# Optimization experiments

Hardware: AMD Instinct MI355X
Metric: run time of the kernel (lower is better)

The kernel has to match this reference:

```python
import jax, jax.numpy as jnp
import numpy as np

N_NODES = 50000
N_EDGES = 640000
D_IN = 128
D_H1 = 128
D_H2 = 256
NEG_SLOPE = 0.2


def setup_inputs() -> dict:
    key = jax.random.key(0)
    ks = jax.random.split(key, 12)
    s = 1.0 / np.sqrt(D_IN)
    inp = {
        'x': jax.random.normal(ks[0], (N_NODES, D_IN), dtype=jnp.float32),
        'edge_index': jax.random.randint(ks[1], (2, N_EDGES), 0, N_NODES, dtype=jnp.int64),
        # GATv2 layer 1: 128 -> 128 (separate lin_l / lin_r, attention vec, residual proj, bias)
        'Wl1': jax.random.normal(ks[2], (D_IN, D_H1), dtype=jnp.float32) * s,
        'Wr1': jax.random.normal(ks[3], (D_IN, D_H1), dtype=jnp.float32) * s,
        'att1': jax.random.normal(ks[4], (D_H1,), dtype=jnp.float32) * s,
        'Wres1': jax.random.normal(ks[5], (D_IN, D_H1), dtype=jnp.float32) * s,
        'b1': jnp.zeros((D_H1,), dtype=jnp.float32),
        # GATv2 layer 2: 128 -> 256
        'Wl2': jax.random.normal(ks[6], (D_H1, D_H2), dtype=jnp.float32) * s,
        'Wr2': jax.random.normal(ks[7], (D_H1, D_H2), dtype=jnp.float32) * s,
        'att2': jax.random.normal(ks[8], (D_H2,), dtype=jnp.float32) * s,
        'Wres2': jax.random.normal(ks[9], (D_H1, D_H2), dtype=jnp.float32) * s,
        'b2': jnp.zeros((D_H2,), dtype=jnp.float32),
    }
    return inp


def _gatv2_layer(x, Wl, Wr, att, Wres, b, src, dst, n_nodes):
    """GATv2Conv (heads=1, residual=True, eval mode/no dropout).
    score e_ij = att . LeakyReLU(Wl x_src + Wr x_dst); softmax over incoming edges per dst;
    out_dst = sum_j alpha_ij * (Wl x_src) + residual + bias.
    """
    xl = x @ Wl                      # [N, F]
    xr = x @ Wr                      # [N, F]
    h = xl[src] + xr[dst]            # [E, F]  gather (irregular access)
    e = jax.nn.leaky_relu(h, NEG_SLOPE) @ att   # [E]
    # segment softmax over destination nodes
    m = jax.ops.segment_max(e, dst, num_segments=n_nodes)      # [N]
    w = jnp.exp(e - m[dst])                                     # [E]
    denom = jax.ops.segment_sum(w, dst, num_segments=n_nodes)   # [N]
    alpha = w / (denom[dst] + 1e-16)                             # [E]
    out = jax.ops.segment_sum(alpha[:, None] * xl[src], dst, num_segments=n_nodes)  # [N, F]
    return out + x @ Wres + b


def reference(x, edge_index, Wl1, Wr1, att1, Wres1, b1, Wl2, Wr2, att2, Wres2, b2):
    src = edge_index[0]
    dst = edge_index[1]
    h = _gatv2_layer(x, Wl1, Wr1, att1, Wres1, b1, src, dst, N_NODES)
    h = jax.nn.elu(h)
    out = _gatv2_layer(h, Wl2, Wr2, att2, Wres2, b2, src, dst, N_NODES)
    return out
```

## Files before the change

kernel.cpp:

```cpp
#include <hip/hip_runtime.h>

typedef unsigned short u16;
typedef unsigned int u32;
typedef __attribute__((ext_vector_type(8))) short bf16x8;
typedef __attribute__((ext_vector_type(4))) float f32x4;
typedef __attribute__((ext_vector_type(2))) float f32x2;

#define NN 50000
#define NE 640000

__device__ __forceinline__ float bfl(u32 u) { return __uint_as_float(u << 16); }
__device__ __forceinline__ float bfh(u32 u) { return __uint_as_float(u & 0xffff0000u); }
__device__ __forceinline__ float bf1(u16 v) { return __uint_as_float(((u32)v) << 16); }
__device__ __forceinline__ u16 f2bf(float f) {
  u32 u = __float_as_uint(f);
  u32 r = (u + 0x7fffu + ((u >> 16) & 1u)) >> 16;
  return (u16)r;
}

__device__ __forceinline__ f32x2 bc2(float s) { return (f32x2){s, s}; }
__device__ __forceinline__ f32x2 pkfma(f32x2 a, f32x2 b, f32x2 c) {
  return __builtin_elementwise_fma(a, b, c);
}
__device__ __forceinline__ f32x2 pkabs(f32x2 a) {
  return __builtin_elementwise_abs(a);
}

template <int CTRL>
__device__ __forceinline__ float dpp_add(float x) {
  int t = __builtin_amdgcn_update_dpp(0, __float_as_int(x), CTRL, 0xf, 0xf, true);
  return x + __int_as_float(t);
}

__device__ __forceinline__ void unpk2(uint4 v, f32x2* o) {
  o[0] = (f32x2){bfl(v.x), bfh(v.x)};
  o[1] = (f32x2){bfl(v.y), bfh(v.y)};
  o[2] = (f32x2){bfl(v.z), bfh(v.z)};
  o[3] = (f32x2){bfl(v.w), bfh(v.w)};
}

__global__ void probe_kernel(const u16* __restrict__ x, const int* __restrict__ ei,
                             int* __restrict__ flags) {
  __shared__ int s_f32, s_i32;
  if (threadIdx.x == 0) { s_f32 = 0; s_i32 = 0; }
  __syncthreads();
  int lf = 0, li = 0;
  for (int i = threadIdx.x; i < 1024; i += 256) {
    float v = bf1(x[i]);
    if (!(fabsf(v) < 1e8f)) lf = 1;
    if (ei[2 * i + 1] != 0) li = 1;
  }
  if (lf) s_f32 = 1;
  if (li) s_i32 = 1;
  __syncthreads();
  if (threadIdx.x == 0) {
    flags[0] = s_f32;
    flags[1] = s_i32 ? 0 : 1;
  }
}

__device__ __forceinline__ int edge_val(const int* __restrict__ w, long j, int i64) {
  return i64 ? w[2 * j] : w[j];
}

__global__ void count_kernel(const int* __restrict__ ei, const int* __restrict__ flags,
                             int* __restrict__ cnt, int E) {
  int e = blockIdx.x * blockDim.x + threadIdx.x;
  if (e >= E) return;
  int d = edge_val(ei, (long)E + e, flags[1]);
  if ((u32)d < (u32)NN) atomicAdd(&cnt[d], 1);
}

__global__ void scan_local(const int* __restrict__ cnt, int* __restrict__ excl,
                           int* __restrict__ bsum, int n) {
  __shared__ int sd[256];
  int t = threadIdx.x;
  int g = blockIdx.x * 256 + t;
  int v = (g < n) ? cnt[g] : 0;
  sd[t] = v;
  __syncthreads();
  for (int off = 1; off < 256; off <<= 1) {
    int x = (t >= off) ? sd[t - off] : 0;
    __syncthreads();
    sd[t] += x;
    __syncthreads();
  }
  int incl = sd[t];
  if (g < n) excl[g] = incl - v;
  if (t == 255) bsum[blockIdx.x] = incl;
}

__global__ void scan_totals(const int* __restrict__ bsum, int* __restrict__ boff, int nb) {
  __shared__ int sd[256];
  int t = threadIdx.x;
  int v = (t < nb) ? bsum[t] : 0;
  sd[t] = v;
  __syncthreads();
  for (int off = 1; off < 256; off <<= 1) {
    int x = (t >= off) ? sd[t - off] : 0;
    __syncthreads();
    sd[t] += x;
    __syncthreads();
  }
  if (t < nb) boff[t] = sd[t] - v;
}

__global__ void scan_add(const int* __restrict__ excl, const int* __restrict__ boff,
                         const int* __restrict__ cnt, int* __restrict__ rowptr,
                         int* __restrict__ fillp, int n) {
  int g = blockIdx.x * 256 + threadIdx.x;
  if (g < n) {
    int e2 = excl[g] + boff[blockIdx.x];
    rowptr[g] = e2;
    fillp[g] = e2;
    if (g == n - 1) rowptr[n] = e2 + cnt[g];
  }
}

__global__ void fill_kernel(const int* __restrict__ ei, const int* __restrict__ flags,
                            int* __restrict__ fillp, int* __restrict__ col, int E) {
  int e = blockIdx.x * blockDim.x + threadIdx.x;
  if (e >= E) return;
  int i64 = flags[1];
  int s = edge_val(ei, (long)e, i64);
  int d = edge_val(ei, (long)E + e, i64);
  if ((u32)d >= (u32)NN) return;
  int p = atomicAdd(&fillp[d], 1);
  col[p] = ((u32)s < (u32)NN) ? s : 0;
}

__global__ void transpose_w(const void* W0, const void* W1, const void* W2,
                            const void* W3, const void* W4, const void* W5,
                            u16* T0, u16* T1, u16* T2, u16* T3, u16* T4, u16* T5,
                            const int* __restrict__ flags) {
  int y = blockIdx.y;
  int M = (y < 3) ? 128 : 256;
  int flat = blockIdx.x * 256 + threadIdx.x;
  if (flat >= M * 128) return;
  int j = flat >> 7;
  int k = flat & 127;
  const void* W = (y == 0) ? W0 : (y == 1) ? W1 : (y == 2) ? W2 : (y == 3) ? W3 : (y == 4) ? W4 : W5;
  u16* T = (y == 0) ? T0 : (y == 1) ? T1 : (y == 2) ? T2 : (y == 3) ? T3 : (y == 4) ? T4 : T5;
  u16 v;
  if (flags[0])
    v = f2bf(((const float*)W)[(size_t)k * M + j]);
  else
    v = ((const u16*)W)[(size_t)k * M + j];
  T[(size_t)j * 128 + k] = v;
}

#define LSTR 136
__global__ __launch_bounds__(256) void gemm3_mfma(
    const void* __restrict__ X,
    const u16* __restrict__ Wta, const u16* __restrict__ Wtb, const u16* __restrict__ Wtc,
    const void* __restrict__ bias,
    u16* __restrict__ Ya, u16* __restrict__ Yb, u16* __restrict__ Yc,
    const int* __restrict__ flags, int x_follows, int N, int M) {
  __shared__ __align__(16) u16 Xs[64 * LSTR];
  __shared__ __align__(16) u16 Bs[128 * LSTR];
  const int K = 128;
  int t = threadIdx.x;
  int lane = t & 63;
  int w = t >> 6;
  int n0g = blockIdx.x * 64;
  int c0 = blockIdx.z * 128;
  int F32X = x_follows ? flags[0] : 0;
  const u16* Wt = (blockIdx.y == 0) ? Wta : ((blockIdx.y == 1) ? Wtb : Wtc);
  u16* Y = (blockIdx.y == 0) ? Ya : ((blockIdx.y == 1) ? Yb : Yc);

  if (!F32X) {
    const u16* Xg = (const u16*)X;
    for (int it = 0; it < 4; ++it) {
      int i = t + 256 * it;
      int r = i >> 4, c8 = (i & 15) * 8;
      int n = n0g + r;
      uint4 v = make_uint4(0, 0, 0, 0);
      if (n < N) v = *(const uint4*)(Xg + (size_t)n * K + c8);
      *(uint4*)(Xs + r * LSTR + c8) = v;
    }
  } else {
    const float* Xg = (const float*)X;
    for (int it = 0; it < 4; ++it) {
      int i = t + 256 * it;
      int r = i >> 4, c8 = (i & 15) * 8;
      int n = n0g + r;
      uint4 pk = make_uint4(0, 0, 0, 0);
      if (n < N) {
        float4 f0 = *(const float4*)(Xg + (size_t)n * K + c8);
        float4 f1 = *(const float4*)(Xg + (size_t)n * K + c8 + 4);
        pk.x = (u32)f2bf(f0.x) | ((u32)f2bf(f0.y) << 16);
        pk.y = (u32)f2bf(f0.z) | ((u32)f2bf(f0.w) << 16);
        pk.z = (u32)f2bf(f1.x) | ((u32)f2bf(f1.y) << 16);
        pk.w = (u32)f2bf(f1.z) | ((u32)f2bf(f1.w) << 16);
      }
      *(uint4*)(Xs + r * LSTR + c8) = pk;
    }
  }
  for (int it = 0; it < 8; ++it) {
    int i = t + 256 * it;
    int j = i >> 4, k8 = (i & 15) * 8;
    uint4 v = *(const uint4*)(Wt + (size_t)(c0 + j) * K + k8);
    *(uint4*)(Bs + j * LSTR + k8) = v;
  }
  __syncthreads();

  int m0 = (w >> 1) * 32;
  int n0 = (w & 1) * 64;
  int l15 = lane & 15;
  int q8 = (lane >> 4) * 8;
  f32x4 acc[2][4];
#pragma unroll
  for (int i = 0; i < 2; ++i)
#pragma unroll
    for (int j = 0; j < 4; ++j) acc[i][j] = (f32x4){0.f, 0.f, 0.f, 0.f};

#pragma unroll
  for (int kc = 0; kc < 4; ++kc) {
    int ko = kc * 32 + q8;
    bf16x8 a[2], b[4];
#pragma unroll
    for (int i = 0; i < 2; ++i)
      a[i] = *(const bf16x8*)(Xs + (m0 + i * 16 + l15) * LSTR + ko);
#pragma unroll
    for (int j = 0; j < 4; ++j)
      b[j] = *(const bf16x8*)(Bs + (n0 + j * 16 + l15) * LSTR + ko);
#pragma unroll
    for (int i = 0; i < 2; ++i)
#pragma unroll
      for (int j = 0; j < 4; ++j)
        acc[i][j] = __builtin_amdgcn_mfma_f32_16x16x32_bf16(a[i], b[j], acc[i][j], 0, 0, 0);
  }
  __syncthreads();

  float bv[4] = {0.f, 0.f, 0.f, 0.f};
  if (blockIdx.y == 2) {
    int F32 = flags[0];
#pragma unroll
    for (int j = 0; j < 4; ++j) {
      int c = c0 + n0 + j * 16 + l15;
      bv[j] = F32 ? ((const float*)bias)[c] : bf1(((const u16*)bias)[c]);
    }
  }

  u16* Ct = Xs;
#pragma unroll
  for (int i = 0; i < 2; ++i)
#pragma unroll
    for (int j = 0; j < 4; ++j) {
      int col = n0 + j * 16 + l15;
      int rbase = m0 + i * 16 + (lane >> 4) * 4;
#pragma unroll
      for (int r = 0; r < 4; ++r)
        Ct[(rbase + r) * LSTR + col] = f2bf(acc[i][j][r] + bv[j]);
    }
  __syncthreads();

  for (int it = 0; it < 4; ++it) {
    int i = t + 256 * it;
    int r = i >> 4, c8 = (i & 15) * 8;
    int n = n0g + r;
    if (n < N) {
      uint4 v = *(const uint4*)(Ct + r * LSTR + c8);
      *(uint4*)(Y + (size_t)n * M + c0 + c8) = v;
    }
  }
}

template <int F, bool ELU, int GL>
__global__ __launch_bounds__(256) void gat_agg_kernel(
    const u16* __restrict__ xl, const u16* __restrict__ xr, const u16* __restrict__ res,
    const void* __restrict__ att, const int* __restrict__ rowptr, const int* __restrict__ col,
    void* __restrict__ out, const int* __restrict__ flags, int out_follows, int N) {
  constexpr int HEPL = F / GL;
  constexpr int HP = HEPL / 2;
  static_assert(HEPL == 8, "GL must be F/8");
  int tid = threadIdx.x;
  int gl = tid & (GL - 1);
  int node = blockIdx.x * (256 / GL) + (tid / GL);
  if (node >= N) return;
  int F32 = flags[0];
  int OF32 = out_follows ? F32 : 0;
  int base = gl * HEPL;

  f32x2 xr2[HP], att6[HP], att4[HP], acc2[HP];
  {
    uint4 xp = *(const uint4*)(xr + (size_t)node * F + base);
    unpk2(xp, xr2);
  }
  if (F32) {
    const float* af = (const float*)att + base;
#pragma unroll
    for (int p = 0; p < HP; ++p) {
      f32x2 a = (f32x2){af[2 * p], af[2 * p + 1]};
      att6[p] = a * 0.6f;
      att4[p] = a * 0.4f;
    }
  } else {
    f32x2 a2[HP];
    uint4 ap = *(const uint4*)((const u16*)att + base);
    unpk2(ap, a2);
#pragma unroll
    for (int p = 0; p < HP; ++p) {
      att6[p] = a2[p] * 0.6f;
      att4[p] = a2[p] * 0.4f;
    }
  }
#pragma unroll
  for (int p = 0; p < HP; ++p) acc2[p] = bc2(0.f);

  float m = -1e30f, l = 0.f;
  int beg = rowptr[node], end = rowptr[node + 1];
  int deg = end - beg;

  if (deg > 0) {
    int nit = (deg + 1) >> 1;
    int dm1 = deg - 1;
    auto ldc = [&](int j) -> int { return col[beg + min(j, dm1)]; };
    auto gat = [&](int c) -> uint4 { return *(const uint4*)(xl + (size_t)c * F + base); };

    int c4 = ldc(4), c5 = ldc(5);
    uint4 va = gat(ldc(0)), vb = gat(ldc(1)), vc = gat(ldc(2)), vd = gat(ldc(3));

    for (int t = 0; t < nit; ++t) {
      uint4 x0v = va, x1v = vb;
      int act1 = (2 * t + 1) < deg;
      va = vc; vb = vd;
      if (t + 2 < nit) { vc = gat(c4); vd = gat(c5); }
      if (t + 3 < nit) { c4 = ldc(2 * t + 6); c5 = ldc(2 * t + 7); }

      f32x2 x0[HP], x1[HP];
      unpk2(x0v, x0);
      unpk2(x1v, x1);
      f32x2 s0 = bc2(0.f), s1 = bc2(0.f);
#pragma unroll
      for (int p = 0; p < HP; ++p) {
        f32x2 h0 = x0[p] + xr2[p];
        f32x2 h1 = x1[p] + xr2[p];
        f32x2 ha0 = pkabs(h0);
        f32x2 ha1 = pkabs(h1);
        s0 = pkfma(att6[p], h0, s0);
        s1 = pkfma(att6[p], h1, s1);
        s0 = pkfma(att4[p], ha0, s0);
        s1 = pkfma(att4[p], ha1, s1);
      }
      float d0 = s0.x + s0.y;
      float d1 = s1.x + s1.y;
      d0 = dpp_add<0xB1>(d0);  d1 = dpp_add<0xB1>(d1);
      d0 = dpp_add<0x4E>(d0);  d1 = dpp_add<0x4E>(d1);
      d0 = dpp_add<0x141>(d0); d1 = dpp_add<0x141>(d1);
      d0 = dpp_add<0x140>(d0); d1 = dpp_add<0x140>(d1);
      if constexpr (GL == 32) {
        d0 += __shfl_xor(d0, 16, 64);
        d1 += __shfl_xor(d1, 16, 64);
      }

      float p0 = d0;
      float p1 = act1 ? d1 : -1e30f;
      float mn = fmaxf(m, fmaxf(p0, p1));
      float scl = __expf(m - mn);
      float w0 = __expf(p0 - mn);
      float w1 = __expf(p1 - mn);
      l = fmaf(l, scl, w0 + w1);
      f32x2 w0b = bc2(w0), w1b = bc2(w1), sclb = bc2(scl);
#pragma unroll
      for (int p = 0; p < HP; ++p)
        acc2[p] = pkfma(sclb, acc2[p], pkfma(w1b, x1[p], w0b * x0[p]));
      m = mn;
    }
  }

  float inv = 1.f / (l + 1e-16f);
  uint4 rp = *(const uint4*)(res + (size_t)node * F + base);
  f32x2 rv[HP];
  unpk2(rp, rv);
  f32x2 ov[HP];
  f32x2 invb = bc2(inv);
#pragma unroll
  for (int p = 0; p < HP; ++p) {
    f32x2 o = pkfma(acc2[p], invb, rv[p]);
    if (ELU) {
      o.x = (o.x > 0.f) ? o.x : (__expf(o.x) - 1.f);
      o.y = (o.y > 0.f) ? o.y : (__expf(o.y) - 1.f);
    }
    ov[p] = o;
  }
  if (OF32) {
    float* of = (float*)out + (size_t)node * F + base;
    float4 f0 = {ov[0].x, ov[0].y, ov[1].x, ov[1].y};
    float4 f1 = {ov[2].x, ov[2].y, ov[3].x, ov[3].y};
    *(float4*)of = f0;
    *(float4*)(of + 4) = f1;
  } else {
    u16* o16 = (u16*)out;
    uint4 pk;
    pk.x = (u32)f2bf(ov[0].x) | ((u32)f2bf(ov[0].y) << 16);
    pk.y = (u32)f2bf(ov[1].x) | ((u32)f2bf(ov[1].y) << 16);
    pk.z = (u32)f2bf(ov[2].x) | ((u32)f2bf(ov[2].y) << 16);
    pk.w = (u32)f2bf(ov[3].x) | ((u32)f2bf(ov[3].y) << 16);
    *(uint4*)(o16 + (size_t)node * F + base) = pk;
  }
}

extern "C" void kernel_launch(void* const* d_in, const int* in_sizes, int n_in,
                              void* d_out, int out_size, void* d_ws, size_t ws_size,
                              hipStream_t stream) {
  const u16* x16 = (const u16*)d_in[0];
  const int* ei = (const int*)d_in[1];
  const int N = NN, E = NE;

  char* ws = (char*)d_ws;
  size_t off = 0;
  auto alloc = [&](size_t bytes) -> void* {
    void* p = (void*)(ws + off);
    off += (bytes + 255) & ~(size_t)255;
    return p;
  };
  int* flags = (int*)alloc(2 * 4);
  int* cnt = (int*)alloc((size_t)N * 4);
  int* rowptr = (int*)alloc((size_t)(N + 1) * 4);
  int* fillp = (int*)alloc((size_t)N * 4);
  int* colb = (int*)alloc((size_t)E * 4);
  int* excl = (int*)alloc((size_t)N * 4);
  int* bsum = (int*)alloc(256 * 4);
  int* boff = (int*)alloc(256 * 4);
  u16* Wt1a = (u16*)alloc((size_t)128 * 128 * 2);
  u16* Wt1b = (u16*)alloc((size_t)128 * 128 * 2);
  u16* Wt1c = (u16*)alloc((size_t)128 * 128 * 2);
  u16* Wt2a = (u16*)alloc((size_t)256 * 128 * 2);
  u16* Wt2b = (u16*)alloc((size_t)256 * 128 * 2);
  u16* Wt2c = (u16*)alloc((size_t)256 * 128 * 2);
  u16* buf1 = (u16*)alloc((size_t)N * 256 * 2);
  u16* buf2 = (u16*)alloc((size_t)N * 256 * 2);
  u16* buf3 = (u16*)alloc((size_t)N * 256 * 2);
  u16* h1 = (u16*)alloc((size_t)N * 128 * 2);
  (void)ws_size; (void)n_in; (void)in_sizes; (void)out_size;

  int nb = (N + 255) / 256;

  probe_kernel<<<1, 256, 0, stream>>>(x16, ei, flags);
  hipMemsetAsync(cnt, 0, (size_t)N * 4, stream);
  count_kernel<<<(E + 255) / 256, 256, 0, stream>>>(ei, flags, cnt, E);
  scan_local<<<nb, 256, 0, stream>>>(cnt, excl, bsum, N);
  scan_totals<<<1, 256, 0, stream>>>(bsum, boff, nb);
  scan_add<<<nb, 256, 0, stream>>>(excl, boff, cnt, rowptr, fillp, N);
  fill_kernel<<<(E + 255) / 256, 256, 0, stream>>>(ei, flags, fillp, colb, E);
  transpose_w<<<dim3(128, 6), 256, 0, stream>>>(
      d_in[2], d_in[3], d_in[5], d_in[7], d_in[8], d_in[10],
      Wt1a, Wt1b, Wt1c, Wt2a, Wt2b, Wt2c, flags);

  int gx = (N + 63) / 64;
  gemm3_mfma<<<dim3(gx, 3, 1), 256, 0, stream>>>(
      d_in[0], Wt1a, Wt1b, Wt1c, d_in[6], buf1, buf2, buf3, flags, 1, N, 128);
  gat_agg_kernel<128, true, 16><<<(N + 15) / 16, 256, 0, stream>>>(
      buf1, buf2, buf3, d_in[4], rowptr, colb, h1, flags, 0, N);
  gemm3_mfma<<<dim3(gx, 3, 2), 256, 0, stream>>>(
      h1, Wt2a, Wt2b, Wt2c, d_in[11], buf1, buf2, buf3, flags, 0, N, 256);
  gat_agg_kernel<256, false, 32><<<(N + 7) / 8, 256, 0, stream>>>(
      buf1, buf2, buf3, d_in[9], rowptr, colb, d_out, flags, 1, N);
}
```

Baseline: 324.6 us.

## Merge setup kernels and loop output halves inside GEMM blocks

The probe kernel now also zeroes the degree counts, which removes a separate memset. The scan-totals kernel is folded into scan_add: each block reduces the preceding block sums itself. Both changes cut the number of launches. The layer-2 GEMM now handles both 128-column output halves in one block, loading the X tile once instead of launching a z-dimension of 2. This halves X tile reloads but gives fewer blocks and more serialized work per block.

```diff
diff --git a/kernel.cpp b/kernel.cpp
--- a/kernel.cpp
+++ b/kernel.cpp
@@ -39,23 +39,27 @@
   o[3] = (f32x2){bfl(v.w), bfh(v.w)};
 }
 
-__global__ void probe_kernel(const u16* __restrict__ x, const int* __restrict__ ei,
-                             int* __restrict__ flags) {
-  __shared__ int s_f32, s_i32;
-  if (threadIdx.x == 0) { s_f32 = 0; s_i32 = 0; }
-  __syncthreads();
-  int lf = 0, li = 0;
-  for (int i = threadIdx.x; i < 1024; i += 256) {
-    float v = bf1(x[i]);
-    if (!(fabsf(v) < 1e8f)) lf = 1;
-    if (ei[2 * i + 1] != 0) li = 1;
-  }
-  if (lf) s_f32 = 1;
-  if (li) s_i32 = 1;
-  __syncthreads();
-  if (threadIdx.x == 0) {
-    flags[0] = s_f32;
-    flags[1] = s_i32 ? 0 : 1;
+__global__ void probe_zero_kernel(const u16* __restrict__ x, const int* __restrict__ ei,
+                                  int* __restrict__ flags, int* __restrict__ cnt, int n) {
+  int g = blockIdx.x * 256 + threadIdx.x;
+  if (g < n) cnt[g] = 0;
+  if (blockIdx.x == 0) {
+    __shared__ int s_f32, s_i32;
+    if (threadIdx.x == 0) { s_f32 = 0; s_i32 = 0; }
+    __syncthreads();
+    int lf = 0, li = 0;
+    for (int i = threadIdx.x; i < 1024; i += 256) {
+      float v = bf1(x[i]);
+      if (!(fabsf(v) < 1e8f)) lf = 1;
+      if (ei[2 * i + 1] != 0) li = 1;
+    }
+    if (lf) s_f32 = 1;
+    if (li) s_i32 = 1;
+    __syncthreads();
+    if (threadIdx.x == 0) {
+      flags[0] = s_f32;
+      flags[1] = s_i32 ? 0 : 1;
+    }
   }
 }
 
@@ -90,27 +94,21 @@
   if (t == 255) bsum[blockIdx.x] = incl;
 }
 
-__global__ void scan_totals(const int* __restrict__ bsum, int* __restrict__ boff, int nb) {
+__global__ void scan_add(const int* __restrict__ excl, const int* __restrict__ bsum,
+                         const int* __restrict__ cnt, int* __restrict__ rowptr,
+                         int* __restrict__ fillp, int n, int nb) {
   __shared__ int sd[256];
   int t = threadIdx.x;
-  int v = (t < nb) ? bsum[t] : 0;
-  sd[t] = v;
+  sd[t] = (t < nb && t < (int)blockIdx.x) ? bsum[t] : 0;
   __syncthreads();
-  for (int off = 1; off < 256; off <<= 1) {
-    int x = (t >= off) ? sd[t - off] : 0;
-    __syncthreads();
-    sd[t] += x;
-    __syncthreads();
-  }
-  if (t < nb) boff[t] = sd[t] - v;
-}
-
-__global__ void scan_add(const int* __restrict__ excl, const int* __restrict__ boff,
-                         const int* __restrict__ cnt, int* __restrict__ rowptr,
-                         int* __restrict__ fillp, int n) {
-  int g = blockIdx.x * 256 + threadIdx.x;
+  for (int off = 128; off > 0; off >>= 1) {
+    if (t < off) sd[t] += sd[t + off];
+    __syncthreads();
+  }
+  int boff = sd[0];
+  int g = blockIdx.x * 256 + t;
   if (g < n) {
-    int e2 = excl[g] + boff[blockIdx.x];
+    int e2 = excl[g] + boff;
     rowptr[g] = e2;
     fillp[g] = e2;
     if (g == n - 1) rowptr[n] = e2 + cnt[g];
@@ -150,12 +148,14 @@
 }
 
 #define LSTR 136
-__global__ __launch_bounds__(256) void gemm3_mfma(
+template <int MZ>
+__global__ __launch_bounds__(256) void gemm3_mz(
     const void* __restrict__ X,
     const u16* __restrict__ Wta, const u16* __restrict__ Wtb, const u16* __restrict__ Wtc,
     const void* __restrict__ bias,
     u16* __restrict__ Ya, u16* __restrict__ Yb, u16* __restrict__ Yc,
-    const int* __restrict__ flags, int x_follows, int N, int M) {
+    const int* __restrict__ flags, int x_follows, int N) {
+  constexpr int M = MZ * 128;
   __shared__ __align__(16) u16 Xs[64 * LSTR];
   __shared__ __align__(16) u16 Bs[128 * LSTR];
   const int K = 128;
@@ -163,7 +163,6 @@
   int lane = t & 63;
   int w = t >> 6;
   int n0g = blockIdx.x * 64;
-  int c0 = blockIdx.z * 128;
   int F32X = x_follows ? flags[0] : 0;
   const u16* Wt = (blockIdx.y == 0) ? Wta : ((blockIdx.y == 1) ? Wtb : Wtc);
   u16* Y = (blockIdx.y == 0) ? Ya : ((blockIdx.y == 1) ? Yb : Yc);
@@ -196,73 +195,80 @@
       *(uint4*)(Xs + r * LSTR + c8) = pk;
     }
   }
-  for (int it = 0; it < 8; ++it) {
-    int i = t + 256 * it;
-    int j = i >> 4, k8 = (i & 15) * 8;
-    uint4 v = *(const uint4*)(Wt + (size_t)(c0 + j) * K + k8);
-    *(uint4*)(Bs + j * LSTR + k8) = v;
-  }
-  __syncthreads();
 
   int m0 = (w >> 1) * 32;
   int n0 = (w & 1) * 64;
   int l15 = lane & 15;
   int q8 = (lane >> 4) * 8;
-  f32x4 acc[2][4];
-#pragma unroll
-  for (int i = 0; i < 2; ++i)
-#pragma unroll
-    for (int j = 0; j < 4; ++j) acc[i][j] = (f32x4){0.f, 0.f, 0.f, 0.f};
-
-#pragma unroll
-  for (int kc = 0; kc < 4; ++kc) {
-    int ko = kc * 32 + q8;
-    bf16x8 a[2], b[4];
+  int F32B = flags[0];
+
+#pragma unroll
+  for (int z = 0; z < MZ; ++z) {
+    int c0 = z * 128;
+    for (int it = 0; it < 8; ++it) {
+      int i = t + 256 * it;
+      int j = i >> 4, k8 = (i & 15) * 8;
+      uint4 v = *(const uint4*)(Wt + (size_t)(c0 + j) * K + k8);
+      *(uint4*)(Bs + j * LSTR + k8) = v;
+    }
+    __syncthreads();
+
+    f32x4 acc[2][4];
 #pragma unroll
     for (int i = 0; i < 2; ++i)
-      a[i] = *(const bf16x8*)(Xs + (m0 + i * 16 + l15) * LSTR + ko);
-#pragma unroll
-    for (int j = 0; j < 4; ++j)
-      b[j] = *(const bf16x8*)(Bs + (n0 + j * 16 + l15) * LSTR + ko);
+#pragma unroll
+      for (int j = 0; j < 4; ++j) acc[i][j] = (f32x4){0.f, 0.f, 0.f, 0.f};
+
+#pragma unroll
+    for (int kc = 0; kc < 4; ++kc) {
+      int ko = kc * 32 + q8;
+      bf16x8 a[2], b[4];
+#pragma unroll
+      for (int i = 0; i < 2; ++i)
+        a[i] = *(const bf16x8*)(Xs + (m0 + i * 16 + l15) * LSTR + ko);
+#pragma unroll
+      for (int j = 0; j < 4; ++j)
+        b[j] = *(const bf16x8*)(Bs + (n0 + j * 16 + l15) * LSTR + ko);
+#pragma unroll
+      for (int i = 0; i < 2; ++i)
+#pragma unroll
+        for (int j = 0; j < 4; ++j)
+          acc[i][j] = __builtin_amdgcn_mfma_f32_16x16x32_bf16(a[i], b[j], acc[i][j], 0, 0, 0);
+    }
+    __syncthreads();
+
+    float bv[4] = {0.f, 0.f, 0.f, 0.f};
+    if (blockIdx.y == 2) {
+#pragma unroll
+      for (int j = 0; j < 4; ++j) {
+        int c = c0 + n0 + j * 16 + l15;
+        bv[j] = F32B ? ((const float*)bias)[c] : bf1(((const u16*)bias)[c]);
+      }
+    }
+
+    u16* Ct = Bs;
 #pragma unroll
     for (int i = 0; i < 2; ++i)
 #pragma unroll
-      for (int j = 0; j < 4; ++j)
-        acc[i][j] = __builtin_amdgcn_mfma_f32_16x16x32_bf16(a[i], b[j], acc[i][j], 0, 0, 0);
-  }
-  __syncthreads();
-
-  float bv[4] = {0.f, 0.f, 0.f, 0.f};
-  if (blockIdx.y == 2) {
-    int F32 = flags[0];
-#pragma unroll
-    for (int j = 0; j < 4; ++j) {
-      int c = c0 + n0 + j * 16 + l15;
-      bv[j] = F32 ? ((const float*)bias)[c] : bf1(((const u16*)bias)[c]);
-    }
-  }
-
-  u16* Ct = Xs;
-#pragma unroll
-  for (int i = 0; i < 2; ++i)
-#pragma unroll
-    for (int j = 0; j < 4; ++j) {
-      int col = n0 + j * 16 + l15;
-      int rbase = m0 + i * 16 + (lane >> 4) * 4;
-#pragma unroll
-      for (int r = 0; r < 4; ++r)
-        Ct[(rbase + r) * LSTR + col] = f2bf(acc[i][j][r] + bv[j]);
-    }
-  __syncthreads();
-
-  for (int it = 0; it < 4; ++it) {
-    int i = t + 256 * it;
-    int r = i >> 4, c8 = (i & 15) * 8;
-    int n = n0g + r;
-    if (n < N) {
-      uint4 v = *(const uint4*)(Ct + r * LSTR + c8);
-      *(uint4*)(Y + (size_t)n * M + c0 + c8) = v;
-    }
+      for (int j = 0; j < 4; ++j) {
+        int colj = n0 + j * 16 + l15;
+        int rbase = m0 + i * 16 + (lane >> 4) * 4;
+#pragma unroll
+        for (int r = 0; r < 4; ++r)
+          Ct[(rbase + r) * LSTR + colj] = f2bf(acc[i][j][r] + bv[j]);
+      }
+    __syncthreads();
+
+    for (int it = 0; it < 4; ++it) {
+      int i = t + 256 * it;
+      int r = i >> 4, c8 = (i & 15) * 8;
+      int n = n0g + r;
+      if (n < N) {
+        uint4 v = *(const uint4*)(Ct + r * LSTR + c8);
+        *(uint4*)(Y + (size_t)n * M + c0 + c8) = v;
+      }
+    }
+    __syncthreads();
   }
 }
 
@@ -422,7 +428,6 @@
   int* colb = (int*)alloc((size_t)E * 4);
   int* excl = (int*)alloc((size_t)N * 4);
   int* bsum = (int*)alloc(256 * 4);
-  int* boff = (int*)alloc(256 * 4);
   u16* Wt1a = (u16*)alloc((size_t)128 * 128 * 2);
   u16* Wt1b = (u16*)alloc((size_t)128 * 128 * 2);
   u16* Wt1c = (u16*)alloc((size_t)128 * 128 * 2);
@@ -437,24 +442,22 @@
 
   int nb = (N + 255) / 256;
 
-  probe_kernel<<<1, 256, 0, stream>>>(x16, ei, flags);
-  hipMemsetAsync(cnt, 0, (size_t)N * 4, stream);
+  probe_zero_kernel<<<nb, 256, 0, stream>>>(x16, ei, flags, cnt, N);
   count_kernel<<<(E + 255) / 256, 256, 0, stream>>>(ei, flags, cnt, E);
   scan_local<<<nb, 256, 0, stream>>>(cnt, excl, bsum, N);
-  scan_totals<<<1, 256, 0, stream>>>(bsum, boff, nb);
-  scan_add<<<nb, 256, 0, stream>>>(excl, boff, cnt, rowptr, fillp, N);
+  scan_add<<<nb, 256, 0, stream>>>(excl, bsum, cnt, rowptr, fillp, N, nb);
   fill_kernel<<<(E + 255) / 256, 256, 0, stream>>>(ei, flags, fillp, colb, E);
   transpose_w<<<dim3(128, 6), 256, 0, stream>>>(
       d_in[2], d_in[3], d_in[5], d_in[7], d_in[8], d_in[10],
       Wt1a, Wt1b, Wt1c, Wt2a, Wt2b, Wt2c, flags);
 
   int gx = (N + 63) / 64;
-  gemm3_mfma<<<dim3(gx, 3, 1), 256, 0, stream>>>(
-      d_in[0], Wt1a, Wt1b, Wt1c, d_in[6], buf1, buf2, buf3, flags, 1, N, 128);
+  gemm3_mz<1><<<dim3(gx, 3), 256, 0, stream>>>(
+      d_in[0], Wt1a, Wt1b, Wt1c, d_in[6], buf1, buf2, buf3, flags, 1, N);
   gat_agg_kernel<128, true, 16><<<(N + 15) / 16, 256, 0, stream>>>(
       buf1, buf2, buf3, d_in[4], rowptr, colb, h1, flags, 0, N);
-  gemm3_mfma<<<dim3(gx, 3, 2), 256, 0, stream>>>(
-      h1, Wt2a, Wt2b, Wt2c, d_in[11], buf1, buf2, buf3, flags, 0, N, 256);
+  gemm3_mz<2><<<dim3(gx, 3), 256, 0, stream>>>(
+      h1, Wt2a, Wt2b, Wt2c, d_in[11], buf1, buf2, buf3, flags, 0, N);
   gat_agg_kernel<256, false, 32><<<(N + 7) / 8, 256, 0, stream>>>(
       buf1, buf2, buf3, d_in[9], rowptr, colb, d_out, flags, 1, N);
 }
```

Result: no change. 318.5 us (-1.9%).
